# Optimization experiments

Hardware: AMD Instinct MI355X
Metric: run time of the kernel (lower is better)

Reference implementation:

```python
import jax, jax.numpy as jnp
import numpy as np

D = 1024
S = 2048
B = 4


def setup_inputs() -> dict:
    key = jax.random.key(0)
    ks = jax.random.split(key, 9)
    sc = 1.0 / np.sqrt(D)
    return {
        "x": jax.random.normal(ks[0], (B, S, D), dtype=jnp.float32),
        "Wq": jax.random.normal(ks[1], (D, D), dtype=jnp.float32) * sc,
        "bq": jax.random.normal(ks[2], (D,), dtype=jnp.float32) * 0.02,
        "Wk": jax.random.normal(ks[3], (D, D), dtype=jnp.float32) * sc,
        "bk": jax.random.normal(ks[4], (D,), dtype=jnp.float32) * 0.02,
        "Wv": jax.random.normal(ks[5], (D, D), dtype=jnp.float32) * sc,
        "bv": jax.random.normal(ks[6], (D,), dtype=jnp.float32) * 0.02,
        "Wp": jax.random.normal(ks[7], (D, D), dtype=jnp.float32) * sc,
        "bp": jax.random.normal(ks[8], (D,), dtype=jnp.float32) * 0.02,
    }


def reference(x, Wq, bq, Wk, bk, Wv, bv, Wp, bp):
    # torch nn.Linear: y = x @ W.T + b  (W stored [out, in])
    q = jnp.einsum("bsd,ed->bse", x, Wq) + bq  # [B,S,D]
    k = jnp.einsum("bsd,ed->bse", x, Wk) + bk
    v = jnp.einsum("bsd,ed->bse", x, Wv) + bv

    scale = 1.0 / jnp.sqrt(jnp.asarray(q.shape[-1], q.dtype))
    # single-head attention: contract over full embd_dim (no head split in source)
    scores = jnp.einsum("bqd,bkd->bqk", q, k) * scale  # [B,S,S]

    seq = x.shape[1]
    causal = jnp.tril(jnp.ones((seq, seq), dtype=bool))  # [S,S]
    scores = jnp.where(causal[None, :, :], scores, -jnp.inf)

    attn = jax.nn.softmax(scores, axis=-1)  # [B,S,S]
    out = jnp.einsum("bqk,bkd->bqd", attn, v)  # [B,S,D]
    out = jnp.einsum("bsd,ed->bse", out, Wp) + bp
    return out
```

## Files before the change

kernel.cpp:

```cpp
#include <hip/hip_runtime.h>

#define AS1(p) ((const __attribute__((address_space(1))) void*)(p))
#define AS3(p) ((__attribute__((address_space(3))) void*)(p))

typedef unsigned short u16;
typedef __bf16 bf16x8 __attribute__((ext_vector_type(8)));
typedef short s16x8 __attribute__((ext_vector_type(8)));
typedef float f32x4 __attribute__((ext_vector_type(4)));
typedef unsigned short u16x4 __attribute__((ext_vector_type(4)));
typedef unsigned short u16x8v __attribute__((ext_vector_type(8)));

__device__ __forceinline__ u16 f2bf(float x) {
    unsigned u = __float_as_uint(x);
    unsigned r = (u + 0x7FFFu + ((u >> 16) & 1u)) >> 16;
    return (u16)r;
}

template <typename V8>
__device__ __forceinline__ auto mfma_sel(V8 a, V8 b, f32x4 c, int)
    -> decltype(__builtin_amdgcn_mfma_f32_16x16x32_bf16(a, b, c, 0, 0, 0))
{
    return __builtin_amdgcn_mfma_f32_16x16x32_bf16(a, b, c, 0, 0, 0);
}
template <typename V8>
__device__ __forceinline__ f32x4 mfma_sel(V8 a, V8 b, f32x4 c, long)
{
    s16x8 a2 = __builtin_bit_cast(s16x8, a);
    s16x8 b2 = __builtin_bit_cast(s16x8, b);
    return __builtin_amdgcn_mfma_f32_16x16x32_bf16(a2, b2, c, 0, 0, 0);
}
__device__ __forceinline__ f32x4 mfma16x16x32(bf16x8 a, bf16x8 b, f32x4 c)
{
    return mfma_sel(a, b, c, 0);
}

__global__ __launch_bounds__(256) void cvt_all_kernel(const float* __restrict__ x,
                                                      const float* __restrict__ Wq,
                                                      const float* __restrict__ Wk,
                                                      const float* __restrict__ Wv,
                                                      const float* __restrict__ Wp,
                                                      u16* __restrict__ xb,
                                                      u16* __restrict__ Wcat,
                                                      u16* __restrict__ Wpb,
                                                      float* __restrict__ rsum,
                                                      int n4x, int n4w, int nrs)
{
    int i = blockIdx.x * 256 + threadIdx.x;
    const int total = n4x + 4 * n4w;
    if (i >= total) {
        int j = i - total;
        if (j < nrs) rsum[j] = 0.f;
        return;
    }
    const float* src;
    u16* dst;
    int off;
    if (i < n4x) {
        src = x; dst = xb; off = i;
    } else {
        int j = i - n4x;
        int w = j >> 18;
        off = j & (n4w - 1);
        src = (w == 0) ? Wq : (w == 1) ? Wk : (w == 2) ? Wv : Wp;
        dst = (w == 3) ? Wpb : (Wcat + (size_t)w * n4w * 4);
    }
    float4 f = ((const float4*)src)[off];
    u16x4 o;
    o.x = f2bf(f.x); o.y = f2bf(f.y); o.z = f2bf(f.z); o.w = f2bf(f.w);
    ((u16x4*)dst)[off] = o;
}

#define MBM 128
#define MBK 64

template <int BIAS, int OUTBF16, int CSKIP, int CKB, int SWZ, int MW,
          int EXPOUT, int RDIV, int PACKA, int FUSET>
__global__ __launch_bounds__(256, MW)
void gemm128(const u16* __restrict__ A, const u16* __restrict__ B,
             void* __restrict__ Cv, const float* __restrict__ bias,
             void* __restrict__ C2, const float* __restrict__ bias2,
             void* __restrict__ C3, const float* __restrict__ bias3,
             float* __restrict__ rsum,
             int M, int N, int K, int lda, int ldb, int ldc,
             long long sA, long long sB, long long sC, float scale)
{
    __shared__ u16 lA[MBM * MBK];
    __shared__ u16 lB[MBM * MBK];

    if (FUSET && blockIdx.z == 4) {
        const u16* vin = (const u16*)C2;
        u16* vout = (u16*)C3;
        u16* tl = lA;
        const int t = threadIdx.x;
        const int r = t >> 2, c4 = (t & 3) << 4;
        const int bid = blockIdx.y * 16 + blockIdx.x;
        for (int it = 0; it < 8; ++it) {
            const int tile = bid * 8 + it;
            const int tc0 = (tile & 15) * 64;
            const int tr0 = (tile >> 4) * 64;
            const u16* src = vin + (size_t)(tr0 + r) * 1024 + tc0 + c4;
            u16x8v a0 = *(const u16x8v*)src;
            u16x8v a1 = *(const u16x8v*)(src + 8);
            #pragma unroll
            for (int j = 0; j < 8; ++j) {
                tl[r * 65 + c4 + j] = a0[j];
                tl[r * 65 + c4 + 8 + j] = a1[j];
            }
            __syncthreads();
            u16x8v b0, b1;
            #pragma unroll
            for (int j = 0; j < 8; ++j) {
                b0[j] = tl[(c4 + j) * 65 + r];
                b1[j] = tl[(c4 + 8 + j) * 65 + r];
            }
            u16* dst = vout + (size_t)(tc0 + r) * 8192 + tr0 + c4;
            *(u16x8v*)dst = b0;
            *(u16x8v*)(dst + 8) = b1;
            __syncthreads();
        }
        return;
    }

    int bx = blockIdx.x, by = blockIdx.y;
    if (SWZ) {
        const int gx = gridDim.x;
        const int nwg = gx * gridDim.y;
        int id = by * gx + bx;
        id = (id & 7) * (nwg >> 3) + (id >> 3);
        bx = id % gx; by = id / gx;
    }
    if (CKB) by = gridDim.y - 1 - by;
    const int m0 = by * MBM;
    const int n0 = bx * MBM;
    if (CSKIP && n0 > m0 + MBM - 1) return;

    const int z = blockIdx.z;
    const int ablk = m0 >> 7;
    long long abase = (long long)z * sA;
    int lda_e = lda;
    if (PACKA) {
        lda_e = (ablk + 1) << 7;
        abase -= (long long)8192 * ablk * (ablk + 1);
    }
    const u16* Ab = A + abase;
    B += (size_t)z * (size_t)sB;

    const int t = threadIdx.x;
    const int lane = t & 63;
    const int w = t >> 6;
    const int wr = w >> 1;
    const int wc = w & 1;
    const int fr = lane & 15, fg = lane >> 4;

    int Keff = K;
    if (CKB) { Keff = m0 + MBM; if (Keff > K) Keff = K; }
    const int nk = Keff / MBK;

    f32x4 acc[4][4] = {};

    for (int kt = 0; kt < nk; ++kt) {
        const int k0 = kt * MBK;
        #pragma unroll
        for (int i = 0; i < 4; ++i) {
            int c = t + i * 256;
            int row = c >> 3;
            int sl = (c & 7) ^ (row & 7);
            __builtin_amdgcn_global_load_lds(
                AS1(Ab + (long long)(m0 + row) * lda_e + k0 + sl * 8),
                AS3(&lA[c * 8]), 16, 0, 0);
            __builtin_amdgcn_global_load_lds(
                AS1(B + (size_t)(n0 + row) * ldb + k0 + sl * 8),
                AS3(&lB[c * 8]), 16, 0, 0);
        }
        __syncthreads();

        #pragma unroll
        for (int kk = 0; kk < MBK; kk += 32) {
            const int cs = (kk >> 3) + fg;
            bf16x8 af[4], bfv[4];
            #pragma unroll
            for (int mi = 0; mi < 4; ++mi) {
                int row = wr * 64 + mi * 16 + fr;
                af[mi] = *(const bf16x8*)&lA[row * 64 + ((cs ^ (row & 7)) << 3)];
            }
            #pragma unroll
            for (int ni = 0; ni < 4; ++ni) {
                int row = wc * 64 + ni * 16 + fr;
                bfv[ni] = *(const bf16x8*)&lB[row * 64 + ((cs ^ (row & 7)) << 3)];
            }
            __builtin_amdgcn_s_setprio(1);
            #pragma unroll
            for (int mi = 0; mi < 4; ++mi)
                #pragma unroll
                for (int ni = 0; ni < 4; ++ni)
                    acc[mi][ni] = mfma16x16x32(af[mi], bfv[ni], acc[mi][ni]);
            __builtin_amdgcn_s_setprio(0);
        }
        __syncthreads();
    }

    if (EXPOUT) {
        const int ldcp = (ablk + 1) << 7;
        u16* Cp = (u16*)Cv + ((long long)z * sC - (long long)8192 * ablk * (ablk + 1));
        float prs[4][4];
        #pragma unroll
        for (int mi = 0; mi < 4; ++mi)
            #pragma unroll
            for (int j = 0; j < 4; ++j) prs[mi][j] = 0.f;
        #pragma unroll
        for (int mi = 0; mi < 4; ++mi) {
            int row0 = m0 + wr * 64 + mi * 16 + fg * 4;
            #pragma unroll
            for (int ni = 0; ni < 4; ++ni) {
                int col = n0 + wc * 64 + ni * 16 + fr;
                #pragma unroll
                for (int j = 0; j < 4; ++j) {
                    int row = row0 + j;
                    float p = (col <= row) ? __expf(acc[mi][ni][j] - 16.f) : 0.f;
                    Cp[(long long)row * ldcp + col] = f2bf(p);
                    prs[mi][j] += p;
                }
            }
        }
        #pragma unroll
        for (int mi = 0; mi < 4; ++mi) {
            #pragma unroll
            for (int j = 0; j < 4; ++j) {
                float s = prs[mi][j];
                s += __shfl_xor(s, 1); s += __shfl_xor(s, 2);
                s += __shfl_xor(s, 4); s += __shfl_xor(s, 8);
                if (fr == 0)
                    atomicAdd(&rsum[(size_t)z * M + m0 + wr * 64 + mi * 16 + fg * 4 + j], s);
            }
        }
        return;
    }

    #pragma unroll
    for (int mi = 0; mi < 4; ++mi) {
        int row0 = m0 + wr * 64 + mi * 16 + fg * 4;
        float invr[4];
        if (RDIV) {
            #pragma unroll
            for (int j = 0; j < 4; ++j)
                invr[j] = 1.f / rsum[(size_t)z * M + row0 + j];
        }
        #pragma unroll
        for (int ni = 0; ni < 4; ++ni) {
            int col = n0 + wc * 64 + ni * 16 + fr;
            if (BIAS == 3) {
                int seg = col >> 10;
                int ccol = col & 1023;
                u16* dst = (seg == 0) ? (u16*)Cv : (seg == 1) ? (u16*)C2 : (u16*)C3;
                float b = ((seg == 0) ? bias : (seg == 1) ? bias2 : bias3)[ccol];
                float sc_ = (seg == 0) ? scale : 1.f;
                #pragma unroll
                for (int j = 0; j < 4; ++j)
                    dst[(size_t)(row0 + j) * 1024 + ccol] =
                        f2bf((acc[mi][ni][j] + b) * sc_);
            } else {
                float bval = (BIAS == 1) ? bias[col] : 0.f;
                #pragma unroll
                for (int j = 0; j < 4; ++j) {
                    float v = RDIV ? acc[mi][ni][j] * invr[j]
                                   : (acc[mi][ni][j] + bval) * scale;
                    size_t off = (size_t)z * (size_t)sC + (size_t)(row0 + j) * ldc + col;
                    if (OUTBF16) ((u16*)Cv)[off] = f2bf(v);
                    else         ((float*)Cv)[off] = v;
                }
            }
        }
    }
}

#define PLDS 81920

template <int BIAS, int OUTBF16>
__global__ __launch_bounds__(256, 2)
void gemm128p(const u16* __restrict__ A, const u16* __restrict__ B,
              void* __restrict__ Cv, const float* __restrict__ bias,
              int M, int N, int K, int lda, int ldb, int ldc, float scale)
{
    extern __shared__ char smem[];

    const int gx = gridDim.x;
    const int nwg = gx * gridDim.y;
    int id = blockIdx.y * gx + blockIdx.x;
    id = (id & 7) * (nwg >> 3) + (id >> 3);
    const int bx = id % gx;
    const int by = id / gx;
    const int m0 = by * MBM;
    const int n0 = bx * MBM;

    const int t = threadIdx.x;
    const int lane = t & 63;
    const int w = t >> 6;
    const int wr = w >> 1, wc = w & 1;
    const int fr = lane & 15, fg = lane >> 4;

    const int nk = K / MBK;

    char* const aB = smem;
    char* const bB = smem + 49152;

    auto STA = [&](int kt, char* dst) {
        const int k0 = kt * MBK;
        #pragma unroll
        for (int i = 0; i < 4; ++i) {
            int c = t + i * 256;
            int row = c >> 3;
            int sl = (c & 7) ^ (row & 7);
            __builtin_amdgcn_global_load_lds(
                AS1(A + (size_t)(m0 + row) * lda + k0 + sl * 8),
                AS3(dst + c * 16), 16, 0, 0);
        }
    };
    auto STB = [&](int kt, char* dst) {
        const int k0 = kt * MBK;
        #pragma unroll
        for (int i = 0; i < 4; ++i) {
            int c = t + i * 256;
            int row = c >> 3;
            int sl = (c & 7) ^ (row & 7);
            __builtin_amdgcn_global_load_lds(
                AS1(B + (size_t)(n0 + row) * ldb + k0 + sl * 8),
                AS3(dst + c * 16), 16, 0, 0);
        }
    };

    f32x4 acc[4][4] = {};

    STA(0, aB);
    STB(0, bB);
    if (nk > 1) {
        STA(1, aB + 16384);
        asm volatile("s_waitcnt vmcnt(4)" ::: "memory");
    } else {
        asm volatile("s_waitcnt vmcnt(0)" ::: "memory");
    }
    __builtin_amdgcn_s_barrier();

    int ca = 0;
    for (int kt = 0; kt < nk; ++kt) {
        if (kt + 1 < nk) STB(kt + 1, bB + ((kt + 1) & 1) * 16384);
        int pa = ca + 2; if (pa >= 3) pa -= 3;
        if (kt + 2 < nk) STA(kt + 2, aB + pa * 16384);

        const char* la = aB + ca * 16384;
        const char* lb = bB + (kt & 1) * 16384;
        #pragma unroll
        for (int kk = 0; kk < MBK; kk += 32) {
            const int cs = (kk >> 3) + fg;
            bf16x8 af[4], bfv[4];
            #pragma unroll
            for (int mi = 0; mi < 4; ++mi) {
                int row = wr * 64 + mi * 16 + fr;
                af[mi] = *(const bf16x8*)(la + row * 128 + ((cs ^ (row & 7)) << 4));
            }
            #pragma unroll
            for (int ni = 0; ni < 4; ++ni) {
                int row = wc * 64 + ni * 16 + fr;
                bfv[ni] = *(const bf16x8*)(lb + row * 128 + ((cs ^ (row & 7)) << 4));
            }
            __builtin_amdgcn_s_setprio(1);
            #pragma unroll
            for (int mi = 0; mi < 4; ++mi)
                #pragma unroll
                for (int ni = 0; ni < 4; ++ni)
                    acc[mi][ni] = mfma16x16x32(af[mi], bfv[ni], acc[mi][ni]);
            __builtin_amdgcn_s_setprio(0);
        }

        if (kt + 2 < nk)      asm volatile("s_waitcnt vmcnt(4)" ::: "memory");
        else if (kt + 1 < nk) asm volatile("s_waitcnt vmcnt(0)" ::: "memory");
        if (kt + 1 < nk) __builtin_amdgcn_s_barrier();
        ++ca; if (ca >= 3) ca = 0;
    }

    #pragma unroll
    for (int mi = 0; mi < 4; ++mi) {
        int row0 = m0 + wr * 64 + mi * 16 + fg * 4;
        #pragma unroll
        for (int ni = 0; ni < 4; ++ni) {
            int col = n0 + wc * 64 + ni * 16 + fr;
            float bval = (BIAS == 1) ? bias[col] : 0.f;
            #pragma unroll
            for (int j = 0; j < 4; ++j) {
                float v = (acc[mi][ni][j] + bval) * scale;
                size_t off = (size_t)(row0 + j) * ldc + col;
                if (OUTBF16) ((u16*)Cv)[off] = f2bf(v);
                else         ((float*)Cv)[off] = v;
            }
        }
    }
}

extern "C" void kernel_launch(void* const* d_in, const int* in_sizes, int n_in,
                              void* d_out, int out_size, void* d_ws, size_t ws_size,
                              hipStream_t stream)
{
    (void)in_sizes; (void)n_in; (void)out_size; (void)ws_size;
    const float* x  = (const float*)d_in[0];
    const float* Wq = (const float*)d_in[1];
    const float* bq = (const float*)d_in[2];
    const float* Wk = (const float*)d_in[3];
    const float* bk = (const float*)d_in[4];
    const float* Wv = (const float*)d_in[5];
    const float* bv = (const float*)d_in[6];
    const float* Wp = (const float*)d_in[7];
    const float* bp = (const float*)d_in[8];

    const int D = 1024, S = 2048, B = 4;
    const int M = B * S;
    const long long sP = 16384LL * 136;

    char* p = (char*)d_ws;
    u16* xb    = (u16*)p; p += (size_t)M * D * 2;
    u16* Wpb   = (u16*)p; p += (size_t)D * D * 2;
    u16* qb    = (u16*)p; p += (size_t)M * D * 2;
    u16* kb    = (u16*)p; p += (size_t)M * D * 2;
    float* rsum = (float*)p; p += (size_t)B * S * 4;
    u16* vb    = (u16*)p; p += (size_t)M * D * 2;
    u16* scp   = (u16*)p;
    u16* Wcat  = scp;
    u16* vTb   = xb;
    u16* attnb = kb;

    const int n4x = M * D / 4;
    const int n4w = D * D / 4;
    const int nrs = B * S;

    hipFuncSetAttribute((const void*)gemm128p<1, 0>,
                        hipFuncAttributeMaxDynamicSharedMemorySize, PLDS);

    cvt_all_kernel<<<(n4x + 4 * n4w + nrs + 255) / 256, 256, 0, stream>>>(
        x, Wq, Wk, Wv, Wp, xb, Wcat, Wpb, rsum, n4x, n4w, nrs);

    gemm128<3, 1, 0, 0, 1, 3, 0, 0, 0, 0><<<dim3(3 * D / MBM, M / MBM), 256, 0, stream>>>(
        xb, Wcat, qb, bq, kb, bk, vb, bv, nullptr,
        M, 3 * D, D, D, D, D, 0, 0, 0, 0.03125f);

    gemm128<0, 1, 1, 0, 0, 4, 1, 0, 0, 1><<<dim3(S / MBM, S / MBM, B + 1), 256, 0, stream>>>(
        qb, kb, scp, nullptr, vb, nullptr, vTb, nullptr, rsum,
        S, S, D, D, D, 0,
        (long long)S * D, (long long)S * D, sP, 1.0f);

    gemm128<0, 1, 0, 1, 0, 4, 0, 1, 1, 0><<<dim3(D / MBM, S / MBM, B), 256, 0, stream>>>(
        scp, vTb, attnb, nullptr, nullptr, nullptr, nullptr, nullptr, rsum,
        S, D, S, 0, M, D,
        sP, (long long)S, (long long)S * D, 1.0f);

    gemm128p<1, 0><<<dim3(D / MBM, M / MBM), 256, PLDS, stream>>>(
        attnb, Wpb, d_out, bp,
        M, D, D, D, D, D, 1.0f);
}
```

Measured before the change: 177.2 us.

## Replace QKV projection GEMM with 256x256-tile 8-wave phased kernel

Adds a dedicated QKV projection kernel that uses 256x256 output tiles, 512 threads and a 128KB double-buffered LDS ring fed by global_load_lds. The K loop is split into four phases, with an MFMA burst per quadrant at raised priority, so that staging of the next tiles overlaps with compute. The larger tile is meant to raise arithmetic intensity and cut global/LDS traffic per FLOP compared with the generic 128x128 gemm128 path. It also removes the BIAS==3 branch from the generic kernel. The grid is 12x32 = 384 workgroups, which means fewer blocks and a possible tail effect, and the 128KB of LDS may limit occupancy to a single workgroup per CU.

After: 181.1 us. 2.2% more time.

```diff
diff --git a/kernel.cpp b/kernel.cpp
--- a/kernel.cpp
+++ b/kernel.cpp
@@ -248,26 +248,14 @@
         #pragma unroll
         for (int ni = 0; ni < 4; ++ni) {
             int col = n0 + wc * 64 + ni * 16 + fr;
-            if (BIAS == 3) {
-                int seg = col >> 10;
-                int ccol = col & 1023;
-                u16* dst = (seg == 0) ? (u16*)Cv : (seg == 1) ? (u16*)C2 : (u16*)C3;
-                float b = ((seg == 0) ? bias : (seg == 1) ? bias2 : bias3)[ccol];
-                float sc_ = (seg == 0) ? scale : 1.f;
-                #pragma unroll
-                for (int j = 0; j < 4; ++j)
-                    dst[(size_t)(row0 + j) * 1024 + ccol] =
-                        f2bf((acc[mi][ni][j] + b) * sc_);
-            } else {
-                float bval = (BIAS == 1) ? bias[col] : 0.f;
-                #pragma unroll
-                for (int j = 0; j < 4; ++j) {
-                    float v = RDIV ? acc[mi][ni][j] * invr[j]
-                                   : (acc[mi][ni][j] + bval) * scale;
-                    size_t off = (size_t)z * (size_t)sC + (size_t)(row0 + j) * ldc + col;
-                    if (OUTBF16) ((u16*)Cv)[off] = f2bf(v);
-                    else         ((float*)Cv)[off] = v;
-                }
+            float bval = (BIAS == 1) ? bias[col] : 0.f;
+            #pragma unroll
+            for (int j = 0; j < 4; ++j) {
+                float v = RDIV ? acc[mi][ni][j] * invr[j]
+                               : (acc[mi][ni][j] + bval) * scale;
+                size_t off = (size_t)z * (size_t)sC + (size_t)(row0 + j) * ldc + col;
+                if (OUTBF16) ((u16*)Cv)[off] = f2bf(v);
+                else         ((float*)Cv)[off] = v;
             }
         }
     }
@@ -393,6 +381,155 @@
             }
         }
     }
+}
+
+#define QLDS2 131072
+
+__global__ __launch_bounds__(512, 2)
+void qkv8ph(const u16* __restrict__ A, const u16* __restrict__ B,
+            u16* __restrict__ q, const float* __restrict__ bq,
+            u16* __restrict__ ko, const float* __restrict__ bk,
+            u16* __restrict__ vo, const float* __restrict__ bv,
+            float qscale)
+{
+    extern __shared__ char smem[];
+
+    const int gx = gridDim.x;
+    const int nwg = gx * gridDim.y;
+    int id = blockIdx.y * gx + blockIdx.x;
+    id = (id & 7) * (nwg >> 3) + (id >> 3);
+    const int bx = id % gx;
+    const int by = id / gx;
+    const int m0 = by * 256;
+    const int n0 = bx * 256;
+
+    const int t = threadIdx.x;
+    const int lane = t & 63;
+    const int w = t >> 6;
+    const int wr = w >> 2;
+    const int wc = w & 3;
+    const int fr = lane & 15, fg = lane >> 4;
+
+    const int nk = 16;
+
+    auto STAGE = [&](int kt, int kind) {
+        if (kt >= nk) return;
+        char* dst = smem + (kt & 1) * 65536 + kind * 16384;
+        const u16* mat = (kind < 2) ? A : B;
+        const int rowbase = (kind < 2) ? (m0 + kind * 128)
+                                       : (n0 + (kind - 2) * 128);
+        const int k0 = kt * 64;
+        #pragma unroll
+        for (int i = 0; i < 2; ++i) {
+            int c = t + i * 512;
+            int lr = c >> 3;
+            int sl = (c & 7) ^ (lr & 7);
+            __builtin_amdgcn_global_load_lds(
+                AS1(mat + (size_t)(rowbase + lr) * 1024 + k0 + sl * 8),
+                AS3(dst + c * 16), 16, 0, 0);
+        }
+    };
+
+    bf16x8 af[8], bfv[4];
+    auto LDA = [&](const char* cb, int mh) {
+        const char* h = cb + mh * 16384;
+        #pragma unroll
+        for (int mi = 0; mi < 4; ++mi) {
+            int lr = wr * 64 + mi * 16 + fr;
+            #pragma unroll
+            for (int ks = 0; ks < 2; ++ks) {
+                int cs = ks * 4 + fg;
+                af[mi * 2 + ks] = *(const bf16x8*)(h + lr * 128 + ((cs ^ (lr & 7)) << 4));
+            }
+        }
+    };
+    auto LDB = [&](const char* cb, int nh) {
+        const char* h = cb + 32768 + nh * 16384;
+        #pragma unroll
+        for (int ni = 0; ni < 2; ++ni) {
+            int lc = wc * 32 + ni * 16 + fr;
+            #pragma unroll
+            for (int ks = 0; ks < 2; ++ks) {
+                int cs = ks * 4 + fg;
+                bfv[ni * 2 + ks] = *(const bf16x8*)(h + lc * 128 + ((cs ^ (lc & 7)) << 4));
+            }
+        }
+    };
+
+    f32x4 acc[2][2][4][2] = {};
+
+#define PH_MFMA(MH, NH)                                                        \
+    asm volatile("s_waitcnt lgkmcnt(0)" ::: "memory");                         \
+    __builtin_amdgcn_sched_barrier(0);                                         \
+    __builtin_amdgcn_s_setprio(1);                                             \
+    _Pragma("unroll")                                                          \
+    for (int mi = 0; mi < 4; ++mi)                                             \
+        _Pragma("unroll")                                                      \
+        for (int ni = 0; ni < 2; ++ni)                                         \
+            _Pragma("unroll")                                                  \
+            for (int ks = 0; ks < 2; ++ks)                                     \
+                acc[MH][NH][mi][ni] =                                          \
+                    mfma16x16x32(af[mi * 2 + ks], bfv[ni * 2 + ks],            \
+                                 acc[MH][NH][mi][ni]);                         \
+    __builtin_amdgcn_s_setprio(0);
+
+    STAGE(0, 2); STAGE(0, 1); STAGE(0, 3); STAGE(0, 0);
+    STAGE(1, 2); STAGE(1, 1); STAGE(1, 3);
+    asm volatile("s_waitcnt vmcnt(6)" ::: "memory");
+    __builtin_amdgcn_s_barrier();
+
+    for (int kt = 0; kt < nk; ++kt) {
+        const char* cb = smem + (kt & 1) * 65536;
+
+        LDA(cb, 0); LDB(cb, 0);
+        STAGE(kt + 1, 0);
+        __builtin_amdgcn_s_barrier();
+        PH_MFMA(0, 0)
+        __builtin_amdgcn_s_barrier();
+
+        LDA(cb, 1);
+        STAGE(kt + 2, 2);
+        __builtin_amdgcn_s_barrier();
+        PH_MFMA(1, 0)
+        __builtin_amdgcn_s_barrier();
+
+        LDB(cb, 1);
+        STAGE(kt + 2, 1);
+        __builtin_amdgcn_s_barrier();
+        PH_MFMA(1, 1)
+        __builtin_amdgcn_s_barrier();
+
+        LDA(cb, 0);
+        STAGE(kt + 2, 3);
+        __builtin_amdgcn_s_barrier();
+        PH_MFMA(0, 1)
+        if (kt + 2 < nk) asm volatile("s_waitcnt vmcnt(6)" ::: "memory");
+        else             asm volatile("s_waitcnt vmcnt(0)" ::: "memory");
+        __builtin_amdgcn_s_barrier();
+    }
+#undef PH_MFMA
+
+    const int seg = n0 >> 10;
+    u16* dst = (seg == 0) ? q : (seg == 1) ? ko : vo;
+    const float* bb = (seg == 0) ? bq : (seg == 1) ? bk : bv;
+    const float sc_ = (seg == 0) ? qscale : 1.f;
+    #pragma unroll
+    for (int mh = 0; mh < 2; ++mh)
+        #pragma unroll
+        for (int nh = 0; nh < 2; ++nh)
+            #pragma unroll
+            for (int mi = 0; mi < 4; ++mi) {
+                int row0 = m0 + mh * 128 + wr * 64 + mi * 16 + fg * 4;
+                #pragma unroll
+                for (int ni = 0; ni < 2; ++ni) {
+                    int ccol = (n0 + nh * 128 + wc * 32 + ni * 16 + fr) & 1023;
+                    float b = bb[ccol];
+                    #pragma unroll
+                    for (int j = 0; j < 4; ++j)
+                        dst[(size_t)(row0 + j) * 1024 + ccol] =
+                            f2bf((acc[mh][nh][mi][ni][j] + b) * sc_);
+                }
+            }
 }
 
 extern "C" void kernel_launch(void* const* d_in, const int* in_sizes, int n_in,
@@ -430,15 +567,16 @@
     const int n4w = D * D / 4;
     const int nrs = B * S;
 
+    hipFuncSetAttribute((const void*)qkv8ph,
+                        hipFuncAttributeMaxDynamicSharedMemorySize, QLDS2);
     hipFuncSetAttribute((const void*)gemm128p<1, 0>,
                         hipFuncAttributeMaxDynamicSharedMemorySize, PLDS);
 
     cvt_all_kernel<<<(n4x + 4 * n4w + nrs + 255) / 256, 256, 0, stream>>>(
         x, Wq, Wk, Wv, Wp, xb, Wcat, Wpb, rsum, n4x, n4w, nrs);
 
-    gemm128<3, 1, 0, 0, 1, 3, 0, 0, 0, 0><<<dim3(3 * D / MBM, M / MBM), 256, 0, stream>>>(
-        xb, Wcat, qb, bq, kb, bk, vb, bv, nullptr,
-        M, 3 * D, D, D, D, D, 0, 0, 0, 0.03125f);
+    qkv8ph<<<dim3(3 * D / 256, M / 256), 512, QLDS2, stream>>>(
+        xb, Wcat, qb, bq, kb, bk, vb, bv, 0.03125f);
 
     gemm128<0, 1, 1, 0, 0, 4, 1, 0, 0, 1><<<dim3(S / MBM, S / MBM, B + 1), 256, 0, stream>>>(
         qb, kb, scp, nullptr, vb, nullptr, vTb, nullptr, rsum,
```
